# Kernel tuning notes

Measured on AMD Instinct MI355X. Metric: run time of the kernel, lower is better.

## Reference

```python
import jax, jax.numpy as jnp
import numpy as np

IN_DIM = 1024
D_QK = IN_DIM // 8  # 128


def setup_inputs() -> dict:
    key = jax.random.key(0)
    ks = jax.random.split(key, 8)
    B, S, H = 8, 2048, IN_DIM
    x = jax.random.normal(ks[0], (B, S, H), dtype=jnp.float32)
    s = 1.0 / np.sqrt(H)
    Wq = jax.random.uniform(ks[1], (H, D_QK), jnp.float32, -s, s)
    bq = jax.random.uniform(ks[2], (D_QK,), jnp.float32, -s, s)
    Wk = jax.random.uniform(ks[3], (H, D_QK), jnp.float32, -s, s)
    bk = jax.random.uniform(ks[4], (D_QK,), jnp.float32, -s, s)
    Wv = jax.random.uniform(ks[5], (H, H), jnp.float32, -s, s)
    bv = jax.random.uniform(ks[6], (H,), jnp.float32, -s, s)
    # nn.Parameter(torch.zeros(1)) in the original; use a small random value so
    # the residual-gated branch is exercised.
    gamma = jax.random.normal(ks[7], (1,), dtype=jnp.float32) * 0.1
    return {"x": x, "Wq": Wq, "bq": bq, "Wk": Wk, "bk": bk,
            "Wv": Wv, "bv": bv, "gamma": gamma}


def reference(x, Wq, bq, Wk, bk, Wv, bv, gamma):
    # x: [B, S, H]
    q = jnp.einsum('bsh,hd->bsd', x, Wq) + bq          # [B, S, D_QK]
    k = jnp.einsum('bsh,hd->bsd', x, Wk) + bk          # [B, S, D_QK]
    v = jnp.einsum('bsh,hg->bsg', x, Wv) + bv          # [B, S, H]
    energy = jnp.einsum('bsd,btd->bst', q, k)          # [B, S, S] (no 1/sqrt(d) scale, as in original)
    attention = jax.nn.softmax(energy, axis=-1)
    out = jnp.einsum('bst,bth->bsh', attention, v)     # [B, S, H]
    return gamma * out + x
```

## Files before the change

### kernel.cpp

```cpp
#include <hip/hip_runtime.h>
#include <hip/hip_bf16.h>
#include <stdint.h>


typedef __attribute__((ext_vector_type(8))) short bf16x8;
typedef __attribute__((ext_vector_type(8))) unsigned short u16x8;
typedef __attribute__((ext_vector_type(4))) float f32x4;

#define S_LEN 2048
#define NB 8
#define HDIM 1024
#define MTOT (NB * S_LEN)
#define NQKV 1280

__device__ __forceinline__ unsigned short f2b(float f) {
  union { float f; unsigned u; } v; v.f = f;
  unsigned u = v.u;
  return (unsigned short)((u + 0x7FFFu + ((u >> 16) & 1u)) >> 16);
}
__device__ __forceinline__ float b2f(unsigned short h) {
  union { unsigned u; float f; } v; v.u = ((unsigned)h) << 16; return v.f;
}

__device__ __forceinline__ void gload16(const void* g, void* l) {
  __builtin_amdgcn_global_load_lds((const __attribute__((address_space(1))) void*)g,
                                   (__attribute__((address_space(3))) void*)l,
                                   16, 0, 0);
}

__device__ __forceinline__ void bar_lgkm() {
  asm volatile("s_waitcnt lgkmcnt(0)" ::: "memory");
  __builtin_amdgcn_sched_barrier(0);
  __builtin_amdgcn_s_barrier();
  __builtin_amdgcn_sched_barrier(0);
}
__device__ __forceinline__ void bar_all() {
  asm volatile("s_waitcnt vmcnt(0) lgkmcnt(0)" ::: "memory");
  __builtin_amdgcn_sched_barrier(0);
  __builtin_amdgcn_s_barrier();
  __builtin_amdgcn_sched_barrier(0);
}

__global__ void k_cast_x(const float* __restrict__ x, unsigned short* __restrict__ xb) {
  int i = blockIdx.x * blockDim.x + threadIdx.x;
  const float4* xv = (const float4*)x;
  float4 a = xv[2 * i], b = xv[2 * i + 1];
  u16x8 o;
  o[0] = f2b(a.x); o[1] = f2b(a.y); o[2] = f2b(a.z); o[3] = f2b(a.w);
  o[4] = f2b(b.x); o[5] = f2b(b.y); o[6] = f2b(b.z); o[7] = f2b(b.w);
  *(u16x8*)(xb + 8 * (size_t)i) = o;
}

__global__ void k_build_w(const float* __restrict__ Wq, const float* __restrict__ bq,
                          const float* __restrict__ Wk, const float* __restrict__ bk,
                          const float* __restrict__ Wv, const float* __restrict__ bv,
                          unsigned short* __restrict__ wt, float* __restrict__ bc) {
  int i = blockIdx.x * 256 + threadIdx.x;
  int n = i >> 10, h = i & 1023;
  float v;
  if (n < 128)      v = Wq[h * 128 + n];
  else if (n < 256) v = Wk[h * 128 + n - 128];
  else              v = Wv[h * 1024 + n - 256];
  wt[i] = f2b(v);
  if (i < NQKV) bc[i] = (i < 128) ? bq[i] : (i < 256) ? bk[i - 128] : bv[i - 256];
}

__launch_bounds__(256, 2)
__global__ void k_gemm_qkv(const unsigned short* __restrict__ A,
                           const unsigned short* __restrict__ Bt,
                           const float* __restrict__ bc,
                           unsigned short* __restrict__ C) {
  __shared__ unsigned short smem[2 * 128 * 32];
  unsigned short* As = smem;
  unsigned short* Bs = smem + 128 * 32;
  const int tid = threadIdx.x;
  const int m0 = blockIdx.x * 128, n0 = blockIdx.y * 128;
  const int l = tid & 63, wid = tid >> 6;
  const int wm = wid >> 1, wn = wid & 1;
  const int l15 = l & 15, lh = l >> 4;
  const int r0 = tid >> 2, seg = tid & 3;
  f32x4 acc[4][4] = {};
  for (int kt = 0; kt < 32; ++kt) {
#pragma unroll
    for (int p = 0; p < 2; ++p) {
      int row = p * 64 + r0;
      gload16(A  + (size_t)(m0 + row) * 1024 + kt * 32 + seg * 8, As + (size_t)(p * 256 + tid) * 8);
      gload16(Bt + (size_t)(n0 + row) * 1024 + kt * 32 + seg * 8, Bs + (size_t)(p * 256 + tid) * 8);
    }
    __syncthreads();
    bf16x8 af[4], bfr[4];
#pragma unroll
    for (int mi = 0; mi < 4; ++mi)
      af[mi] = *(const bf16x8*)&As[(wm * 64 + mi * 16 + l15) * 32 + 8 * lh];
#pragma unroll
    for (int ni = 0; ni < 4; ++ni)
      bfr[ni] = *(const bf16x8*)&Bs[(wn * 64 + ni * 16 + l15) * 32 + 8 * lh];
#pragma unroll
    for (int mi = 0; mi < 4; ++mi)
#pragma unroll
      for (int ni = 0; ni < 4; ++ni)
        acc[mi][ni] = __builtin_amdgcn_mfma_f32_16x16x32_bf16(af[mi], bfr[ni], acc[mi][ni], 0, 0, 0);
    __syncthreads();
  }
  unsigned short* sc = As + wid * 1024;
  const int erow = l >> 2, ech = l & 3;
  for (int mi = 0; mi < 4; ++mi) {
    asm volatile("s_waitcnt lgkmcnt(0)" ::: "memory");
#pragma unroll
    for (int ni = 0; ni < 4; ++ni) {
      float bias = bc[n0 + wn * 64 + ni * 16 + l15];
#pragma unroll
      for (int r = 0; r < 4; ++r) {
        int row = lh * 4 + r;
        int col = (ni * 16 + l15) ^ ((row & 7) * 8);
        sc[row * 64 + col] = f2b(acc[mi][ni][r] + bias);
      }
    }
    asm volatile("s_waitcnt lgkmcnt(0)" ::: "memory");
    int gr = m0 + wm * 64 + mi * 16 + erow;
#pragma unroll
    for (int h = 0; h < 2; ++h) {
      int ch = ech + h * 4;
      int colsw = (ch ^ (erow & 7)) * 8;
      u16x8 vv = *(const u16x8*)(sc + erow * 64 + colsw);
      *(u16x8*)(&C[(size_t)gr * NQKV + n0 + wn * 64 + ch * 8]) = vv;
    }
  }
}

__global__ void k_transpose_v(const unsigned short* __restrict__ qkv, unsigned short* __restrict__ vt) {
  __shared__ unsigned short t[64][66];
  const int m0 = blockIdx.x * 64, c0 = blockIdx.y * 64;
  const int tx = threadIdx.x & 63, ty = threadIdx.x >> 6;
#pragma unroll
  for (int i = 0; i < 64; i += 4)
    t[ty + i][tx] = qkv[(size_t)(m0 + ty + i) * NQKV + 256 + c0 + tx];
  __syncthreads();
#pragma unroll
  for (int i = 0; i < 64; i += 4)
    vt[(size_t)(c0 + ty + i) * MTOT + m0 + tx] = t[tx][ty + i];
}

#define POOL_BYTES 125952
#define QS_OFF   0
#define PS_OFF   32768
#define PM_OFF   32768
#define PL_OFF   36864
#define SM_OFF   43008
#define SGL_OFF  43520
#define KA0_OFF  44032
#define KA1_OFF  76800
#define KB0_OFF  44032
#define KB1_OFF  52224
#define V0_OFF   60416
#define V1_OFF   93184

__launch_bounds__(512, 2)
__global__ void k_attn(const unsigned short* __restrict__ qkv,
                       const unsigned short* __restrict__ vt,
                       const float* __restrict__ x,
                       const float* __restrict__ gamma,
                       float* __restrict__ out) {
  __shared__ alignas(16) char pool[POOL_BYTES];
  const int tid = threadIdx.x;
  const int l = tid & 63, w = tid >> 6;
  const int l15 = l & 15, lh = l >> 4;
  int flat = (int)blockIdx.x + ((int)blockIdx.y << 4) + ((int)blockIdx.z << 5);
  int nf_ = ((flat & 7) << 5) + (flat >> 3);
  const int b = nf_ >> 5, nh = (nf_ >> 4) & 1, mt = nf_ & 15;
  const int m0 = mt << 7;
  const size_t rowbase = (size_t)b * S_LEN;

  unsigned short* Qs = (unsigned short*)(pool + QS_OFF);
  unsigned short* Ps = (unsigned short*)(pool + PS_OFF);
  float* pm  = (float*)(pool + PM_OFF);
  float* pl  = (float*)(pool + PL_OFF);
  float* sm  = (float*)(pool + SM_OFF);
  float* sgl = (float*)(pool + SGL_OFF);

#pragma unroll
  for (int j = 0; j < 4; ++j) {
    int f = j * 512 + tid;
    int qr = f >> 4, c = f & 15;
    gload16(qkv + (rowbase + m0 + qr) * NQKV + ((c ^ (qr & 7)) * 8),
            (void*)(pool + QS_OFF + f * 16));
  }
#pragma unroll
  for (int j = 0; j < 4; ++j) {
    int f = j * 512 + tid;
    int kr = f >> 4, c = f & 15;
    gload16(qkv + (rowbase + kr) * NQKV + 128 + ((c ^ (kr & 7)) * 8),
            (void*)(pool + KA0_OFF + f * 16));
  }
  bar_all();

  float m_p[8], l_p[8];
#pragma unroll
  for (int i = 0; i < 8; ++i) { m_p[i] = -3e38f; l_p[i] = 0.f; }

  for (int kt = 0; kt < 16; ++kt) {
    const char* ka = pool + ((kt & 1) ? KA1_OFF : KA0_OFF);
    if (kt < 15) {
      char* dst = pool + ((kt & 1) ? KA0_OFF : KA1_OFF);
#pragma unroll
      for (int j = 0; j < 4; ++j) {
        int f = j * 512 + tid;
        int kr = f >> 4, c = f & 15;
        gload16(qkv + (rowbase + (size_t)(kt + 1) * 128 + kr) * NQKV + 128 + ((c ^ (kr & 7)) * 8),
                (void*)(dst + f * 16));
      }
    }
    bf16x8 kaf[4];
#pragma unroll
    for (int ds = 0; ds < 4; ++ds)
      kaf[ds] = *(const bf16x8*)(ka + ((w * 16 + l15) * 128 + (((ds * 4 + lh) ^ (l15 & 7)) * 8)) * 2);
#pragma unroll
    for (int qf = 0; qf < 8; ++qf) {
      f32x4 e = {};
#pragma unroll
      for (int ds = 0; ds < 4; ++ds) {
        bf16x8 qb = *(const bf16x8*)(Qs + (qf * 16 + l15) * 128 + (((ds * 4 + lh) ^ (l15 & 7)) * 8));
        e = __builtin_amdgcn_mfma_f32_16x16x32_bf16(kaf[ds], qb, e, 0, 0, 0);
      }
      float mx = fmaxf(fmaxf(e[0], e[1]), fmaxf(e[2], e[3]));
      if (mx > m_p[qf]) { l_p[qf] *= __expf(m_p[qf] - mx); m_p[qf] = mx; }
      l_p[qf] += __expf(e[0] - m_p[qf]) + __expf(e[1] - m_p[qf]) +
                 __expf(e[2] - m_p[qf]) + __expf(e[3] - m_p[qf]);
    }
    bar_all();
  }
#pragma unroll
  for (int qf = 0; qf < 8; ++qf) {
    float m = m_p[qf], ls = l_p[qf];
    {
      float om = __shfl_xor(m, 16), ol = __shfl_xor(ls, 16);
      float M = fmaxf(m, om);
      ls = ls * __expf(m - M) + ol * __expf(om - M); m = M;
    }
    {
      float om = __shfl_xor(m, 32), ol = __shfl_xor(ls, 32);
      float M = fmaxf(m, om);
      ls = ls * __expf(m - M) + ol * __expf(om - M); m = M;
    }
    if (l < 16) { pm[w * 128 + qf * 16 + l] = m; pl[w * 128 + qf * 16 + l] = ls; }
  }
  bar_lgkm();
  if (tid < 128) {
    float g0 = gamma[0];
    float M = -3e38f, L = 0.f;
#pragma unroll
    for (int ww = 0; ww < 8; ++ww) {
      float om = pm[ww * 128 + tid], ol = pl[ww * 128 + tid];
      float M2 = fmaxf(M, om);
      L = L * __expf(M - M2) + ol * __expf(om - M2);
      M = M2;
    }
    sm[tid] = M; sgl[tid] = g0 / L;
  }
  bar_lgkm();

  float m_r[4];
#pragma unroll
  for (int r = 0; r < 4; ++r) m_r[r] = sm[w * 16 + lh * 4 + r];

  const size_t vtk = (size_t)b * S_LEN;
  auto stageB = [&](int kt, int p) {
    char* kb = pool + (p ? KB1_OFF : KB0_OFF);
    char* vb = pool + (p ? V1_OFF : V0_OFF);
    {
      int key = tid >> 4, c = tid & 15;
      gload16(qkv + (rowbase + (size_t)kt * 32 + key) * NQKV + 128 + ((c ^ (key & 7)) * 8),
              (void*)(kb + tid * 16));
    }
#pragma unroll
    for (int j = 0; j < 4; ++j) {
      int f = j * 512 + tid;
      int ww = f >> 8, nl = (f >> 2) & 63, kc = f & 3;
      gload16(vt + (size_t)(nh * 512 + ww * 64 + nl) * MTOT + vtk + kt * 32 + ((kc ^ (nl & 3)) * 8),
              (void*)(vb + f * 16));
    }
  };

  stageB(0, 0);
  bar_all();
  f32x4 acc[8][4] = {};
  for (int kt = 0; kt < 64; ++kt) {
    int p = kt & 1;
    const unsigned short* kb = (const unsigned short*)(pool + (p ? KB1_OFF : KB0_OFF));
    const unsigned short* vb = (const unsigned short*)(pool + (p ? V1_OFF : V0_OFF));
    if (kt < 63) stageB(kt + 1, p ^ 1);
    f32x4 s0 = {}, s1 = {};
#pragma unroll
    for (int ds = 0; ds < 4; ++ds) {
      int ch = ((ds * 4 + lh) ^ (l15 & 7)) * 8;
      bf16x8 aq = *(const bf16x8*)(Qs + (w * 16 + l15) * 128 + ch);
      bf16x8 k0 = *(const bf16x8*)(kb + l15 * 128 + ch);
      bf16x8 k1 = *(const bf16x8*)(kb + (16 + l15) * 128 + ch);
      s0 = __builtin_amdgcn_mfma_f32_16x16x32_bf16(aq, k0, s0, 0, 0, 0);
      s1 = __builtin_amdgcn_mfma_f32_16x16x32_bf16(aq, k1, s1, 0, 0, 0);
    }
#pragma unroll
    for (int r = 0; r < 4; ++r) {
      Ps[(w * 16 + lh * 4 + r) * 40 + l15]      = f2b(__expf(s0[r] - m_r[r]));
      Ps[(w * 16 + lh * 4 + r) * 40 + 16 + l15] = f2b(__expf(s1[r] - m_r[r]));
    }
    bar_lgkm();
    bf16x8 vf[4];
#pragma unroll
    for (int nf = 0; nf < 4; ++nf)
      vf[nf] = *(const bf16x8*)(vb + w * 2048 + (nf * 16 + l15) * 32 + ((lh ^ (l15 & 3)) * 8));
#pragma unroll
    for (int mi = 0; mi < 8; ++mi) {
      bf16x8 pa = *(const bf16x8*)(Ps + (mi * 16 + l15) * 40 + lh * 8);
#pragma unroll
      for (int nf = 0; nf < 4; ++nf)
        acc[mi][nf] = __builtin_amdgcn_mfma_f32_16x16x32_bf16(pa, vf[nf], acc[mi][nf], 0, 0, 0);
    }
    bar_all();
  }

  float* sc = (float*)(pool + V0_OFF) + w * 1088;
  const int row16 = l >> 2, c4 = l & 3;
#pragma unroll
  for (int mi = 0; mi < 8; ++mi) {
    asm volatile("s_waitcnt lgkmcnt(0)" ::: "memory");
    __builtin_amdgcn_sched_barrier(0);
#pragma unroll
    for (int nf = 0; nf < 4; ++nf)
#pragma unroll
      for (int r = 0; r < 4; ++r)
        sc[(lh * 4 + r) * 68 + nf * 16 + l15] = acc[mi][nf][r];
    asm volatile("s_waitcnt lgkmcnt(0)" ::: "memory");
    __builtin_amdgcn_sched_barrier(0);
    float scl = sgl[mi * 16 + row16];
    size_t grow = rowbase + m0 + mi * 16 + row16;
#pragma unroll
    for (int g = 0; g < 4; ++g) {
      int ch = c4 + g * 4;
      f32x4 v = *(const f32x4*)(sc + row16 * 68 + ch * 4);
      size_t o = grow * 1024 + (size_t)(nh * 512 + w * 64 + ch * 4);
      float4 xv = *(const float4*)(x + o);
      float4 ov;
      ov.x = scl * v[0] + xv.x; ov.y = scl * v[1] + xv.y;
      ov.z = scl * v[2] + xv.z; ov.w = scl * v[3] + xv.w;
      *(float4*)(out + o) = ov;
    }
  }
}

extern "C" void kernel_launch(void* const* d_in, const int* in_sizes, int n_in,
                              void* d_out, int out_size, void* d_ws, size_t ws_size,
                              hipStream_t stream) {
  const float* x     = (const float*)d_in[0];
  const float* Wq    = (const float*)d_in[1];
  const float* bq    = (const float*)d_in[2];
  const float* Wk    = (const float*)d_in[3];
  const float* bk    = (const float*)d_in[4];
  const float* Wv    = (const float*)d_in[5];
  const float* bv    = (const float*)d_in[6];
  const float* gamma = (const float*)d_in[7];
  float* out = (float*)d_out;
  char* ws = (char*)d_ws;

  unsigned short* xb  = (unsigned short*)(ws);
  unsigned short* wt  = (unsigned short*)(ws + 33554432);
  float*          bc  = (float*)         (ws + 36175872);
  unsigned short* qkv = (unsigned short*)(ws + 36180992);
  unsigned short* vt  = xb;

  hipLaunchKernelGGL(k_cast_x,      dim3(8192),      dim3(256), 0, stream, x, xb);
  hipLaunchKernelGGL(k_build_w,     dim3(5120),      dim3(256), 0, stream, Wq, bq, Wk, bk, Wv, bv, wt, bc);
  hipLaunchKernelGGL(k_gemm_qkv,    dim3(128, 10),   dim3(256), 0, stream, xb, wt, bc, qkv);
  hipLaunchKernelGGL(k_transpose_v, dim3(256, 16),   dim3(256), 0, stream, qkv, vt);
  hipLaunchKernelGGL(k_attn,        dim3(16, 2, 8),  dim3(512), 0, stream, qkv, vt, x, gamma, out);
}
```

Baseline: 343.5 us.

## Load K and V directly into registers in attention, double 1024-thread blocks

```diff
diff --git a/kernel.cpp b/kernel.cpp
--- a/kernel.cpp
+++ b/kernel.cpp
@@ -141,21 +141,16 @@
     vt[(size_t)(c0 + ty + i) * MTOT + m0 + tx] = t[tx][ty + i];
 }
 
-#define POOL_BYTES 125952
+#define POOL_BYTES 70656
 #define QS_OFF   0
-#define PS_OFF   32768
-#define PM_OFF   32768
-#define PL_OFF   36864
-#define SM_OFF   43008
-#define SGL_OFF  43520
-#define KA0_OFF  44032
-#define KA1_OFF  76800
-#define KB0_OFF  44032
-#define KB1_OFF  52224
-#define V0_OFF   60416
-#define V1_OFF   93184
-
-__launch_bounds__(512, 2)
+#define PS0_OFF  32768
+#define PS1_OFF  43008
+#define PM_OFF   53248
+#define PL_OFF   61440
+#define SM_OFF   69632
+#define SGL_OFF  70144
+
+__launch_bounds__(1024, 4)
 __global__ void k_attn(const unsigned short* __restrict__ qkv,
                        const unsigned short* __restrict__ vt,
                        const float* __restrict__ x,
@@ -172,62 +167,50 @@
   const size_t rowbase = (size_t)b * S_LEN;
 
   unsigned short* Qs = (unsigned short*)(pool + QS_OFF);
-  unsigned short* Ps = (unsigned short*)(pool + PS_OFF);
   float* pm  = (float*)(pool + PM_OFF);
   float* pl  = (float*)(pool + PL_OFF);
   float* sm  = (float*)(pool + SM_OFF);
   float* sgl = (float*)(pool + SGL_OFF);
 
 #pragma unroll
-  for (int j = 0; j < 4; ++j) {
-    int f = j * 512 + tid;
+  for (int j = 0; j < 2; ++j) {
+    int f = j * 1024 + tid;
     int qr = f >> 4, c = f & 15;
     gload16(qkv + (rowbase + m0 + qr) * NQKV + ((c ^ (qr & 7)) * 8),
             (void*)(pool + QS_OFF + f * 16));
   }
-#pragma unroll
-  for (int j = 0; j < 4; ++j) {
-    int f = j * 512 + tid;
-    int kr = f >> 4, c = f & 15;
-    gload16(qkv + (rowbase + kr) * NQKV + 128 + ((c ^ (kr & 7)) * 8),
-            (void*)(pool + KA0_OFF + f * 16));
-  }
   bar_all();
 
   float m_p[8], l_p[8];
 #pragma unroll
   for (int i = 0; i < 8; ++i) { m_p[i] = -3e38f; l_p[i] = 0.f; }
 
-  for (int kt = 0; kt < 16; ++kt) {
-    const char* ka = pool + ((kt & 1) ? KA1_OFF : KA0_OFF);
-    if (kt < 15) {
-      char* dst = pool + ((kt & 1) ? KA0_OFF : KA1_OFF);
-#pragma unroll
-      for (int j = 0; j < 4; ++j) {
-        int f = j * 512 + tid;
-        int kr = f >> 4, c = f & 15;
-        gload16(qkv + (rowbase + (size_t)(kt + 1) * 128 + kr) * NQKV + 128 + ((c ^ (kr & 7)) * 8),
-                (void*)(dst + f * 16));
-      }
-    }
-    bf16x8 kaf[4];
-#pragma unroll
-    for (int ds = 0; ds < 4; ++ds)
-      kaf[ds] = *(const bf16x8*)(ka + ((w * 16 + l15) * 128 + (((ds * 4 + lh) ^ (l15 & 7)) * 8)) * 2);
+  const unsigned short* kbase = qkv + (rowbase + w * 16 + l15) * NQKV + 128 + lh * 8;
+  bf16x8 kc[4];
+#pragma unroll
+  for (int ds = 0; ds < 4; ++ds) kc[ds] = *(const bf16x8*)(kbase + ds * 32);
+  for (int kt = 0; kt < 8; ++kt) {
+    bf16x8 kn[4];
+    if (kt < 7) {
+      const unsigned short* kb2 = kbase + (size_t)(kt + 1) * 256 * NQKV;
+#pragma unroll
+      for (int ds = 0; ds < 4; ++ds) kn[ds] = *(const bf16x8*)(kb2 + ds * 32);
+    }
 #pragma unroll
     for (int qf = 0; qf < 8; ++qf) {
       f32x4 e = {};
 #pragma unroll
       for (int ds = 0; ds < 4; ++ds) {
         bf16x8 qb = *(const bf16x8*)(Qs + (qf * 16 + l15) * 128 + (((ds * 4 + lh) ^ (l15 & 7)) * 8));
-        e = __builtin_amdgcn_mfma_f32_16x16x32_bf16(kaf[ds], qb, e, 0, 0, 0);
+        e = __builtin_amdgcn_mfma_f32_16x16x32_bf16(kc[ds], qb, e, 0, 0, 0);
       }
       float mx = fmaxf(fmaxf(e[0], e[1]), fmaxf(e[2], e[3]));
       if (mx > m_p[qf]) { l_p[qf] *= __expf(m_p[qf] - mx); m_p[qf] = mx; }
       l_p[qf] += __expf(e[0] - m_p[qf]) + __expf(e[1] - m_p[qf]) +
                  __expf(e[2] - m_p[qf]) + __expf(e[3] - m_p[qf]);
     }
-    bar_all();
+#pragma unroll
+    for (int ds = 0; ds < 4; ++ds) kc[ds] = kn[ds];
   }
 #pragma unroll
   for (int qf = 0; qf < 8; ++qf) {
@@ -249,7 +232,7 @@
     float g0 = gamma[0];
     float M = -3e38f, L = 0.f;
 #pragma unroll
-    for (int ww = 0; ww < 8; ++ww) {
+    for (int ww = 0; ww < 16; ++ww) {
       float om = pm[ww * 128 + tid], ol = pl[ww * 128 + tid];
       float M2 = fmaxf(M, om);
       L = L * __expf(M - M2) + ol * __expf(om - M2);
@@ -259,86 +242,58 @@
   }
   bar_lgkm();
 
+  const int rt = w >> 1, kf = w & 1;
   float m_r[4];
 #pragma unroll
-  for (int r = 0; r < 4; ++r) m_r[r] = sm[w * 16 + lh * 4 + r];
-
-  const size_t vtk = (size_t)b * S_LEN;
-  auto stageB = [&](int kt, int p) {
-    char* kb = pool + (p ? KB1_OFF : KB0_OFF);
-    char* vb = pool + (p ? V1_OFF : V0_OFF);
-    {
-      int key = tid >> 4, c = tid & 15;
-      gload16(qkv + (rowbase + (size_t)kt * 32 + key) * NQKV + 128 + ((c ^ (key & 7)) * 8),
-              (void*)(kb + tid * 16));
-    }
-#pragma unroll
-    for (int j = 0; j < 4; ++j) {
-      int f = j * 512 + tid;
-      int ww = f >> 8, nl = (f >> 2) & 63, kc = f & 3;
-      gload16(vt + (size_t)(nh * 512 + ww * 64 + nl) * MTOT + vtk + kt * 32 + ((kc ^ (nl & 3)) * 8),
-              (void*)(vb + f * 16));
-    }
-  };
-
-  stageB(0, 0);
-  bar_all();
-  f32x4 acc[8][4] = {};
+  for (int r = 0; r < 4; ++r) m_r[r] = sm[rt * 16 + lh * 4 + r];
+
+  const unsigned short* kqbase = qkv + (rowbase + kf * 16 + l15) * NQKV + 128 + lh * 8;
+  const unsigned short* vbase  = vt + (size_t)(nh * 512 + w * 32 + l15) * MTOT + rowbase + lh * 8;
+
+  f32x4 acc[8][2] = {};
   for (int kt = 0; kt < 64; ++kt) {
-    int p = kt & 1;
-    const unsigned short* kb = (const unsigned short*)(pool + (p ? KB1_OFF : KB0_OFF));
-    const unsigned short* vb = (const unsigned short*)(pool + (p ? V1_OFF : V0_OFF));
-    if (kt < 63) stageB(kt + 1, p ^ 1);
-    f32x4 s0 = {}, s1 = {};
+    unsigned short* Pw = (unsigned short*)(pool + ((kt & 1) ? PS1_OFF : PS0_OFF));
+    bf16x8 vf0 = *(const bf16x8*)(vbase + (size_t)kt * 32);
+    bf16x8 vf1 = *(const bf16x8*)(vbase + (size_t)16 * MTOT + (size_t)kt * 32);
+    f32x4 s = {};
 #pragma unroll
     for (int ds = 0; ds < 4; ++ds) {
-      int ch = ((ds * 4 + lh) ^ (l15 & 7)) * 8;
-      bf16x8 aq = *(const bf16x8*)(Qs + (w * 16 + l15) * 128 + ch);
-      bf16x8 k0 = *(const bf16x8*)(kb + l15 * 128 + ch);
-      bf16x8 k1 = *(const bf16x8*)(kb + (16 + l15) * 128 + ch);
-      s0 = __builtin_amdgcn_mfma_f32_16x16x32_bf16(aq, k0, s0, 0, 0, 0);
-      s1 = __builtin_amdgcn_mfma_f32_16x16x32_bf16(aq, k1, s1, 0, 0, 0);
-    }
-#pragma unroll
-    for (int r = 0; r < 4; ++r) {
-      Ps[(w * 16 + lh * 4 + r) * 40 + l15]      = f2b(__expf(s0[r] - m_r[r]));
-      Ps[(w * 16 + lh * 4 + r) * 40 + 16 + l15] = f2b(__expf(s1[r] - m_r[r]));
-    }
+      bf16x8 aq = *(const bf16x8*)(Qs + (rt * 16 + l15) * 128 + (((ds * 4 + lh) ^ (l15 & 7)) * 8));
+      bf16x8 kb = *(const bf16x8*)(kqbase + (size_t)kt * 32 * NQKV + ds * 32);
+      s = __builtin_amdgcn_mfma_f32_16x16x32_bf16(aq, kb, s, 0, 0, 0);
+    }
+#pragma unroll
+    for (int r = 0; r < 4; ++r)
+      Pw[(rt * 16 + lh * 4 + r) * 40 + kf * 16 + l15] = f2b(__expf(s[r] - m_r[r]));
     bar_lgkm();
-    bf16x8 vf[4];
-#pragma unroll
-    for (int nf = 0; nf < 4; ++nf)
-      vf[nf] = *(const bf16x8*)(vb + w * 2048 + (nf * 16 + l15) * 32 + ((lh ^ (l15 & 3)) * 8));
 #pragma unroll
     for (int mi = 0; mi < 8; ++mi) {
-      bf16x8 pa = *(const bf16x8*)(Ps + (mi * 16 + l15) * 40 + lh * 8);
-#pragma unroll
-      for (int nf = 0; nf < 4; ++nf)
-        acc[mi][nf] = __builtin_amdgcn_mfma_f32_16x16x32_bf16(pa, vf[nf], acc[mi][nf], 0, 0, 0);
-    }
-    bar_all();
-  }
-
-  float* sc = (float*)(pool + V0_OFF) + w * 1088;
-  const int row16 = l >> 2, c4 = l & 3;
+      bf16x8 pa = *(const bf16x8*)(Pw + (mi * 16 + l15) * 40 + lh * 8);
+      acc[mi][0] = __builtin_amdgcn_mfma_f32_16x16x32_bf16(pa, vf0, acc[mi][0], 0, 0, 0);
+      acc[mi][1] = __builtin_amdgcn_mfma_f32_16x16x32_bf16(pa, vf1, acc[mi][1], 0, 0, 0);
+    }
+  }
+
+  float* sc = (float*)pool + w * 576;
+  const int erow = l >> 2, ech = l & 3;
 #pragma unroll
   for (int mi = 0; mi < 8; ++mi) {
     asm volatile("s_waitcnt lgkmcnt(0)" ::: "memory");
     __builtin_amdgcn_sched_barrier(0);
 #pragma unroll
-    for (int nf = 0; nf < 4; ++nf)
+    for (int nf = 0; nf < 2; ++nf)
 #pragma unroll
       for (int r = 0; r < 4; ++r)
-        sc[(lh * 4 + r) * 68 + nf * 16 + l15] = acc[mi][nf][r];
+        sc[(lh * 4 + r) * 36 + nf * 16 + l15] = acc[mi][nf][r];
     asm volatile("s_waitcnt lgkmcnt(0)" ::: "memory");
     __builtin_amdgcn_sched_barrier(0);
-    float scl = sgl[mi * 16 + row16];
-    size_t grow = rowbase + m0 + mi * 16 + row16;
-#pragma unroll
-    for (int g = 0; g < 4; ++g) {
-      int ch = c4 + g * 4;
-      f32x4 v = *(const f32x4*)(sc + row16 * 68 + ch * 4);
-      size_t o = grow * 1024 + (size_t)(nh * 512 + w * 64 + ch * 4);
+    float scl = sgl[mi * 16 + erow];
+    size_t grow = rowbase + m0 + mi * 16 + erow;
+#pragma unroll
+    for (int h = 0; h < 2; ++h) {
+      int ch = ech + h * 4;
+      f32x4 v = *(const f32x4*)(sc + erow * 36 + ch * 4);
+      size_t o = grow * 1024 + (size_t)(nh * 512 + w * 32 + ch * 4);
       float4 xv = *(const float4*)(x + o);
       float4 ov;
       ov.x = scl * v[0] + xv.x; ov.y = scl * v[1] + xv.y;
@@ -368,9 +323,9 @@
   unsigned short* qkv = (unsigned short*)(ws + 36180992);
   unsigned short* vt  = xb;
 
-  hipLaunchKernelGGL(k_cast_x,      dim3(8192),      dim3(256), 0, stream, x, xb);
-  hipLaunchKernelGGL(k_build_w,     dim3(5120),      dim3(256), 0, stream, Wq, bq, Wk, bk, Wv, bv, wt, bc);
-  hipLaunchKernelGGL(k_gemm_qkv,    dim3(128, 10),   dim3(256), 0, stream, xb, wt, bc, qkv);
-  hipLaunchKernelGGL(k_transpose_v, dim3(256, 16),   dim3(256), 0, stream, qkv, vt);
-  hipLaunchKernelGGL(k_attn,        dim3(16, 2, 8),  dim3(512), 0, stream, qkv, vt, x, gamma, out);
-}
+  hipLaunchKernelGGL(k_cast_x,      dim3(8192),      dim3(256),  0, stream, x, xb);
+  hipLaunchKernelGGL(k_build_w,     dim3(5120),      dim3(256),  0, stream, Wq, bq, Wk, bk, Wv, bv, wt, bc);
+  hipLaunchKernelGGL(k_gemm_qkv,    dim3(128, 10),   dim3(256),  0, stream, xb, wt, bc, qkv);
+  hipLaunchKernelGGL(k_transpose_v, dim3(256, 16),   dim3(256),  0, stream, qkv, vt);
+  hipLaunchKernelGGL(k_attn,        dim3(16, 2, 8),  dim3(1024), 0, stream, qkv, vt, x, gamma, out);
+}
```

Result: slower. 513.3 us (+49.4%).
